# Performance work log

Measured on AMD Instinct MI355X. Metric: run time of the kernel, lower is better.

The kernel has to match this reference:

```python
import jax, jax.numpy as jnp
import numpy as np

H, HKV, DH = 32, 8, 128
ROPE_BASE = 500000.0


def _rope(x, pos):
    # x: [B, H, T, D]; MLX non-traditional rope (split halves)
    D = x.shape[-1]
    half = D // 2
    freqs = ROPE_BASE ** (-(jnp.arange(half, dtype=jnp.float32) * 2.0 / D))  # [half]
    t = pos + jnp.arange(x.shape[2], dtype=jnp.float32)                      # [T]
    ang = t[:, None] * freqs[None, :]                                        # [T, half]
    cos, sin = jnp.cos(ang), jnp.sin(ang)
    x1, x2 = x[..., :half], x[..., half:]
    return jnp.concatenate([x1 * cos - x2 * sin, x1 * sin + x2 * cos], axis=-1)


def setup_inputs() -> dict:
    key = jax.random.key(0)
    ks = jax.random.split(key, 5)
    B, T, HID = 1, 2048, 4096
    s = 0.02
    return {
        "hidden_states": jax.random.normal(ks[0], (B, T, HID), jnp.float32),
        "Wq": jax.random.normal(ks[1], (H * DH, HID), jnp.float32) * s,
        "Wk": jax.random.normal(ks[2], (HKV * DH, HID), jnp.float32) * s,
        "Wv": jax.random.normal(ks[3], (HKV * DH, HID), jnp.float32) * s,
        "Wo": jax.random.normal(ks[4], (HID, H * DH), jnp.float32) * s,
        "k_cache": jnp.zeros((1, HKV, 4096, DH), jnp.float32),
        "v_cache": jnp.zeros((1, HKV, 4096, DH), jnp.float32),
        "pos_int": 0,
    }


def reference(hidden_states, Wq, Wk, Wv, Wo, k_cache, v_cache, pos_int):
    B, T, _ = hidden_states.shape
    # QKV projections (no bias, Llama-style) -> [B, h, T, D]
    q = (hidden_states @ Wq.T).reshape(B, T, H, DH).transpose(0, 2, 1, 3)
    k = (hidden_states @ Wk.T).reshape(B, T, HKV, DH).transpose(0, 2, 1, 3)
    v = (hidden_states @ Wv.T).reshape(B, T, HKV, DH).transpose(0, 2, 1, 3)
    # RoPE with position offset
    q = _rope(q, pos_int)
    k = _rope(k, pos_int)
    # KV-cache scatter update at pos_int, then window to [:pos_int+T]
    k_cache = jax.lax.dynamic_update_slice(k_cache, k, (0, 0, pos_int, 0))
    v_cache = jax.lax.dynamic_update_slice(v_cache, v, (0, 0, pos_int, 0))
    Tk = pos_int + T
    k_win = k_cache[:, :, :Tk, :]
    v_win = v_cache[:, :, :Tk, :]
    # GQA: repeat_interleave KV heads to match query heads
    group = H // HKV
    k_ = jnp.repeat(k_win, group, axis=1)   # [B, H, Tk, D]
    v_ = jnp.repeat(v_win, group, axis=1)
    # SDPA, is_causal=True => top-left aligned causal mask (query i sees keys j<=i)
    scale = 1.0 / jnp.sqrt(jnp.asarray(DH, jnp.float32))
    scores = jnp.einsum("bhtd,bhsd->bhts", q, k_) * scale  # [B, H, T, Tk]
    causal = jnp.arange(Tk)[None, :] <= jnp.arange(T)[:, None]
    scores = jnp.where(causal[None, None], scores, jnp.finfo(scores.dtype).min)
    attn = jax.nn.softmax(scores, axis=-1)
    out = jnp.einsum("bhts,bhsd->bhtd", attn, v_)           # [B, H, T, D]
    out = out.transpose(0, 2, 1, 3).reshape(B, T, H * DH)
    return out @ Wo.T
```

## Files before the change

kernel.cpp:

```cpp
#include <hip/hip_runtime.h>


#define DEVI __device__ __forceinline__

typedef __attribute__((ext_vector_type(8))) short short8;
typedef __attribute__((ext_vector_type(4))) float f32x4;

DEVI unsigned short f2bf(float f) {
  union { float f; unsigned u; } x; x.f = f;
  unsigned r = x.u + 0x7FFFu + ((x.u >> 16) & 1u);
  return (unsigned short)(r >> 16);
}
DEVI float bf2f(unsigned short h) {
  union { unsigned u; float f; } x; x.u = ((unsigned)h) << 16;
  return x.f;
}
DEVI f32x4 mfma16(short8 a, short8 b, f32x4 c) {
  return __builtin_amdgcn_mfma_f32_16x16x32_bf16(a, b, c, 0, 0, 0);
}
DEVI void gl2lds16(const unsigned short* g, unsigned short* l) {
  __builtin_amdgcn_global_load_lds(
      (const __attribute__((address_space(1))) unsigned int*)g,
      (__attribute__((address_space(3))) unsigned int*)l, 16, 0, 0);
}
DEVI void bar() { __builtin_amdgcn_s_barrier(); }
DEVI void sfence() { __builtin_amdgcn_sched_barrier(0); }

__global__ __launch_bounds__(256)
void cvt_kernel(const float* __restrict__ src, unsigned short* __restrict__ dst,
                int n4) {
  int i = blockIdx.x * 256 + threadIdx.x;
  const int stride = gridDim.x * 256;
  for (; i < n4; i += stride) {
    float4 v = ((const float4*)src)[i];
    ushort4 h;
    h.x = f2bf(v.x); h.y = f2bf(v.y); h.z = f2bf(v.z); h.w = f2bf(v.w);
    ((ushort4*)dst)[i] = h;
  }
}

__global__ __launch_bounds__(512, 2)
void gemm_qkv_8ph(const unsigned short* __restrict__ hsb,
                  const unsigned short* __restrict__ Wqb,
                  const unsigned short* __restrict__ Wkb,
                  const unsigned short* __restrict__ Wvb,
                  unsigned short* __restrict__ Qb,
                  unsigned short* __restrict__ Kb,
                  unsigned short* __restrict__ Vb) {
  const int K = 4096;
  const int NT = 64;
  __shared__ __align__(16) unsigned short Ls[2][2][2][256][32];
  const int tid = threadIdx.x, lane = tid & 63, w = tid >> 6;
  const int wr = w >> 2, wc = w & 3;
  const int m0 = blockIdx.y * 256;
  const int n0g = blockIdx.x * 256;

  const unsigned short* Bsrc; unsigned short* outp; int ldo, oc;
  if (n0g < 4096)      { Bsrc = Wqb + (size_t)n0g * K;          outp = Qb; ldo = 4096; oc = n0g; }
  else if (n0g < 5120) { Bsrc = Wkb + (size_t)(n0g - 4096) * K; outp = Kb; ldo = 1024; oc = n0g - 4096; }
  else                 { Bsrc = Wvb + (size_t)(n0g - 5120) * K; outp = Vb; ldo = 1024; oc = n0g - 5120; }
  const unsigned short* Asrc = hsb + (size_t)m0 * K;

  auto stageU = [&](const unsigned short* src, int ab, int kh, int tt, int bb) {
#pragma unroll
    for (int j = 0; j < 2; ++j) {
      const int seg = j * 8 + w;
      const int row = seg * 16 + (lane >> 2);
      const int cs  = (lane & 3) ^ ((row >> 1) & 3);
      gl2lds16(src + (size_t)row * K + tt * 64 + kh * 32 + cs * 8,
               &Ls[bb][ab][kh][seg * 16][0]);
    }
  };
  auto ldA = [&](int bb, int kh, int fm) -> short8 {
    const int ra = wr * 128 + fm * 16 + (lane & 15);
    const int cs = (lane >> 4) ^ ((ra >> 1) & 3);
    return *(const short8*)&Ls[bb][0][kh][ra][cs * 8];
  };
  auto ldB = [&](int bb, int kh, int fn) -> short8 {
    const int rb = wc * 64 + fn * 16 + (lane & 15);
    const int cs = (lane >> 4) ^ ((rb >> 1) & 3);
    return *(const short8*)&Ls[bb][1][kh][rb][cs * 8];
  };

  f32x4 acc[8][4];
#pragma unroll
  for (int i = 0; i < 8; ++i)
#pragma unroll
    for (int j = 0; j < 4; ++j) acc[i][j] = (f32x4){0.f, 0.f, 0.f, 0.f};

  stageU(Asrc, 0, 0, 0, 0);
  stageU(Asrc, 0, 1, 0, 0);
  stageU(Bsrc, 1, 0, 0, 0);
  stageU(Bsrc, 1, 1, 0, 0);
  stageU(Bsrc, 1, 0, 1, 1);
  stageU(Asrc, 0, 0, 1, 1);
  stageU(Bsrc, 1, 1, 1, 1);
  asm volatile("s_waitcnt vmcnt(6)" ::: "memory");
  bar();
  sfence();

  short8 af[4], bfr[4];
  for (int t = 0; t < NT; ++t) {
    const int bb = t & 1, nb = bb ^ 1;
#pragma unroll
    for (int i = 0; i < 4; ++i) af[i] = ldA(bb, 0, i);
#pragma unroll
    for (int i = 0; i < 4; ++i) bfr[i] = ldB(bb, 0, i);
    if (t + 1 < NT) stageU(Asrc, 0, 1, t + 1, nb);
    bar();
    __builtin_amdgcn_s_setprio(1);
#pragma unroll
    for (int i = 0; i < 4; ++i)
#pragma unroll
      for (int j = 0; j < 4; ++j) acc[i][j] = mfma16(af[i], bfr[j], acc[i][j]);
    __builtin_amdgcn_s_setprio(0);
    sfence(); bar(); sfence();
#pragma unroll
    for (int i = 0; i < 4; ++i) af[i] = ldA(bb, 0, 4 + i);
    if (t + 2 < NT) stageU(Bsrc, 1, 0, t + 2, bb);
    bar();
    __builtin_amdgcn_s_setprio(1);
#pragma unroll
    for (int i = 0; i < 4; ++i)
#pragma unroll
      for (int j = 0; j < 4; ++j) acc[4 + i][j] = mfma16(af[i], bfr[j], acc[4 + i][j]);
    __builtin_amdgcn_s_setprio(0);
    sfence(); bar(); sfence();
#pragma unroll
    for (int i = 0; i < 4; ++i) af[i] = ldA(bb, 1, i);
#pragma unroll
    for (int i = 0; i < 4; ++i) bfr[i] = ldB(bb, 1, i);
    if (t + 2 < NT) stageU(Asrc, 0, 0, t + 2, bb);
    bar();
    __builtin_amdgcn_s_setprio(1);
#pragma unroll
    for (int i = 0; i < 4; ++i)
#pragma unroll
      for (int j = 0; j < 4; ++j) acc[i][j] = mfma16(af[i], bfr[j], acc[i][j]);
    __builtin_amdgcn_s_setprio(0);
    sfence(); bar(); sfence();
#pragma unroll
    for (int i = 0; i < 4; ++i) af[i] = ldA(bb, 1, 4 + i);
    if (t + 2 < NT) stageU(Bsrc, 1, 1, t + 2, bb);
    bar();
    __builtin_amdgcn_s_setprio(1);
#pragma unroll
    for (int i = 0; i < 4; ++i)
#pragma unroll
      for (int j = 0; j < 4; ++j) acc[4 + i][j] = mfma16(af[i], bfr[j], acc[4 + i][j]);
    __builtin_amdgcn_s_setprio(0);
    if (t < NT - 2) asm volatile("s_waitcnt vmcnt(6)" ::: "memory");
    else            asm volatile("s_waitcnt vmcnt(0)" ::: "memory");
    sfence(); bar(); sfence();
  }

#pragma unroll
  for (int fm = 0; fm < 8; ++fm) {
    const int rb0 = m0 + wr * 128 + fm * 16 + ((lane >> 4) << 2);
#pragma unroll
    for (int fn = 0; fn < 4; ++fn) {
      const int cb = oc + wc * 64 + fn * 16 + (lane & 15);
#pragma unroll
      for (int r = 0; r < 4; ++r)
        outp[(size_t)(rb0 + r) * ldo + cb] = f2bf(acc[fm][fn][r]);
    }
  }
}

__global__ __launch_bounds__(256)
void transpose_v(const unsigned short* __restrict__ Vb,
                 unsigned short* __restrict__ VtG) {
  __shared__ unsigned short tile[64][68];
  const int tid = threadIdx.x;
  const int t0 = blockIdx.x * 64;
  const int c0 = blockIdx.y * 64;
  const int r = tid >> 4;
  const int c4 = (tid & 15) << 2;
#pragma unroll
  for (int i = 0; i < 4; ++i) {
    ushort4 v = *(const ushort4*)(Vb + (size_t)(t0 + r + i * 16) * 1024 + c0 + c4);
    *(ushort4*)&tile[r + i * 16][c4] = v;
  }
  __syncthreads();
#pragma unroll
  for (int i = 0; i < 4; ++i) {
    int d = r + i * 16;
    ushort4 o;
    o.x = tile[c4 + 0][d]; o.y = tile[c4 + 1][d];
    o.z = tile[c4 + 2][d]; o.w = tile[c4 + 3][d];
    *(ushort4*)(VtG + (size_t)(c0 + d) * 2048 + t0 + c4) = o;
  }
}

__global__ __launch_bounds__(256)
void rope_kernel(unsigned short* __restrict__ Qb, unsigned short* __restrict__ Kb,
                 const int* __restrict__ posp) {
  const int QP = 2048 * 32 * 64;
  const int KP = 2048 * 8 * 64;
  int idx = blockIdx.x * 256 + threadIdx.x;
  if (idx >= QP + KP) return;
  unsigned short* base; int t, hh, d, ld;
  if (idx < QP) {
    base = Qb; ld = 4096;
    t = idx >> 11; int rem = idx & 2047; hh = rem >> 6; d = rem & 63;
  } else {
    int j = idx - QP; base = Kb; ld = 1024;
    t = j >> 9; int rem = j & 511; hh = rem >> 6; d = rem & 63;
  }
  float freq = exp2f(-(float)d * 0.29580575880077f);
  float ang = (float)(t + posp[0]) * freq;
  float s, c;
  __sincosf(ang, &s, &c);
  size_t i1 = (size_t)t * ld + hh * 128 + d;
  float x1 = bf2f(base[i1]), x2 = bf2f(base[i1 + 64]);
  base[i1]      = f2bf(x1 * c - x2 * s);
  base[i1 + 64] = f2bf(x1 * s + x2 * c);
}

__global__ __launch_bounds__(512, 4)
void attn_kernel(const unsigned short* __restrict__ Qb,
                 const unsigned short* __restrict__ Kb,
                 const unsigned short* __restrict__ VtG,
                 unsigned short* __restrict__ Ob) {
  __shared__ __align__(16) unsigned short Ks[64][128];
  __shared__ __align__(16) unsigned short Vt[128][64];
  __shared__ __align__(16) unsigned short Ps[8][16][64];
  const int tid = threadIdx.x, lane = tid & 63, w = tid >> 6;
  const int h = blockIdx.y;
  const int qt = (blockIdx.y >> 4) ? (15 - blockIdx.x) : blockIdx.x;
  const int kh = h >> 2;
  const int q0 = qt * 128;
  const float SCALE = 0.08838834764831845f;

  short8 aq[4];
  {
    const int qrow = q0 + w * 16 + (lane & 15);
#pragma unroll
    for (int ks = 0; ks < 4; ++ks)
      aq[ks] = *(const short8*)(Qb + (size_t)qrow * 4096 + h * 128 + ks * 32 +
                                ((lane >> 4) << 3));
  }

  f32x4 o_acc[8];
#pragma unroll
  for (int n8 = 0; n8 < 8; ++n8) o_acc[n8] = (f32x4){0.f, 0.f, 0.f, 0.f};
  float mst[4], lst[4];
#pragma unroll
  for (int r = 0; r < 4; ++r) { mst[r] = -1e30f; lst[r] = 0.f; }

  const int ksrow0 = w * 8 + (lane >> 4);
  const int vdrow0 = w * 16 + (lane >> 3);

  const int ntiles = 2 * (qt + 1);
  for (int st = 0; st < ntiles; ++st) {
    const int s0 = st * 64;
#pragma unroll
    for (int j = 0; j < 2; ++j) {
      int sr = ksrow0 + j * 4;
      int sc = (((lane & 15) << 4) ^ ((sr & 7) << 4)) >> 1;
      gl2lds16(Kb + (size_t)(s0 + sr) * 1024 + kh * 128 + sc, &Ks[w * 8 + j * 4][0]);
    }
#pragma unroll
    for (int j = 0; j < 2; ++j) {
      int dr = vdrow0 + j * 8;
      int sc = (((lane & 7) << 4) ^ ((dr & 7) << 4)) >> 1;
      gl2lds16(VtG + (size_t)(kh * 128 + dr) * 2048 + s0 + sc, &Vt[w * 16 + j * 8][0]);
    }
    __syncthreads();

    f32x4 sacc[4];
#pragma unroll
    for (int ni = 0; ni < 4; ++ni) sacc[ni] = (f32x4){0.f, 0.f, 0.f, 0.f};
#pragma unroll
    for (int ks = 0; ks < 4; ++ks) {
      const int co = ks * 64 + ((lane >> 4) << 4);
      short8 bk[4];
#pragma unroll
      for (int ni = 0; ni < 4; ++ni) {
        int kr = ni * 16 + (lane & 15);
        bk[ni] = *(const short8*)((const char*)(&Ks[kr][0]) + (co ^ ((kr & 7) << 4)));
      }
#pragma unroll
      for (int ni = 0; ni < 4; ++ni)
        sacc[ni] = mfma16(aq[ks], bk[ni], sacc[ni]);
    }

    char* pb = (char*)(&Ps[w][0][0]);
#pragma unroll
    for (int r = 0; r < 4; ++r) {
      const int qrow = q0 + w * 16 + ((lane >> 4) << 2) + r;
      float v4[4]; float vmax = -1e30f;
#pragma unroll
      for (int ni = 0; ni < 4; ++ni) {
        int scol = s0 + ni * 16 + (lane & 15);
        float x = sacc[ni][r] * SCALE;
        if (scol > qrow) x = -1e30f;
        v4[ni] = x; vmax = fmaxf(vmax, x);
      }
      vmax = fmaxf(vmax, __shfl_xor(vmax, 1));
      vmax = fmaxf(vmax, __shfl_xor(vmax, 2));
      vmax = fmaxf(vmax, __shfl_xor(vmax, 4));
      vmax = fmaxf(vmax, __shfl_xor(vmax, 8));
      float mo = mst[r];
      float mn = fmaxf(mo, vmax);
      float al = __expf(mo - mn);
      float rs = 0.f;
      const int prow = ((lane >> 4) << 2) + r;
      const int pswz = ((prow >> 2) & 3) << 5;
#pragma unroll
      for (int ni = 0; ni < 4; ++ni) {
        float p = __expf(v4[ni] - mn);
        rs += p;
        int cbyte = (ni * 16 + (lane & 15)) * 2;
        *(unsigned short*)(pb + prow * 128 + (cbyte ^ pswz)) = f2bf(p);
      }
      rs += __shfl_xor(rs, 1);
      rs += __shfl_xor(rs, 2);
      rs += __shfl_xor(rs, 4);
      rs += __shfl_xor(rs, 8);
      lst[r] = lst[r] * al + rs;
      mst[r] = mn;
#pragma unroll
      for (int n8 = 0; n8 < 8; ++n8) o_acc[n8][r] *= al;
    }

#pragma unroll
    for (int ks2 = 0; ks2 < 2; ++ks2) {
      const int co = ks2 * 64 + ((lane >> 4) << 4);
      const int pr = lane & 15;
      short8 pa = *(const short8*)(pb + pr * 128 + (co ^ (((pr >> 2) & 3) << 5)));
#pragma unroll
      for (int n8 = 0; n8 < 8; ++n8) {
        int vr = n8 * 16 + (lane & 15);
        short8 bv = *(const short8*)((const char*)(&Vt[vr][0]) + (co ^ ((vr & 7) << 4)));
        o_acc[n8] = mfma16(pa, bv, o_acc[n8]);
      }
    }
    __syncthreads();
  }

#pragma unroll
  for (int r = 0; r < 4; ++r) {
    float inv = 1.0f / lst[r];
    int row = q0 + w * 16 + ((lane >> 4) << 2) + r;
#pragma unroll
    for (int n8 = 0; n8 < 8; ++n8)
      Ob[(size_t)row * 4096 + h * 128 + n8 * 16 + (lane & 15)] =
          f2bf(o_acc[n8][r] * inv);
  }
}

__global__ __launch_bounds__(256, 2)
void gemm_out_bf16(const unsigned short* __restrict__ Ab,
                   const unsigned short* __restrict__ Wob,
                   float* __restrict__ Cout) {
  const int K = 4096;
  __shared__ __align__(16) unsigned short As[128][64];
  __shared__ __align__(16) unsigned short Bs[128][64];
  const int tid = threadIdx.x, lane = tid & 63, wid = tid >> 6;
  const int m0 = blockIdx.y * 128;
  const int n0 = blockIdx.x * 128;
  const unsigned short* Asrc = Ab + (size_t)m0 * K;
  const unsigned short* Bsrc = Wob + (size_t)n0 * K;

  f32x4 acc[4][4];
#pragma unroll
  for (int i = 0; i < 4; ++i)
#pragma unroll
    for (int j = 0; j < 4; ++j) acc[i][j] = (f32x4){0.f, 0.f, 0.f, 0.f};

  const int wm = (wid >> 1) * 64, wn = (wid & 1) * 64;
  const int srow = wid * 32 + (lane >> 3);
  const int scol = (lane & 7) * 8;

  for (int k0 = 0; k0 < K; k0 += 64) {
#pragma unroll
    for (int i = 0; i < 4; ++i) {
      gl2lds16(Asrc + (size_t)(srow + i * 8) * K + k0 + scol, &As[wid * 32 + i * 8][0]);
      gl2lds16(Bsrc + (size_t)(srow + i * 8) * K + k0 + scol, &Bs[wid * 32 + i * 8][0]);
    }
    __syncthreads();
#pragma unroll
    for (int ks = 0; ks < 2; ++ks) {
      short8 af[4], bfr[4];
      const int co = ks * 64 + ((lane >> 4) << 4);
#pragma unroll
      for (int i = 0; i < 4; ++i) {
        af[i]  = *(const short8*)((const char*)(&As[wm + i * 16 + (lane & 15)][0]) + co);
        bfr[i] = *(const short8*)((const char*)(&Bs[wn + i * 16 + (lane & 15)][0]) + co);
      }
#pragma unroll
      for (int i = 0; i < 4; ++i)
#pragma unroll
        for (int j = 0; j < 4; ++j)
          acc[i][j] = mfma16(af[i], bfr[j], acc[i][j]);
    }
    __syncthreads();
  }

#pragma unroll
  for (int i = 0; i < 4; ++i) {
    int rb = m0 + wm + i * 16 + ((lane >> 4) << 2);
#pragma unroll
    for (int j = 0; j < 4; ++j) {
      int cb = n0 + wn + j * 16 + (lane & 15);
#pragma unroll
      for (int r = 0; r < 4; ++r)
        Cout[(size_t)(rb + r) * 4096 + cb] = acc[i][j][r];
    }
  }
}

extern "C" void kernel_launch(void* const* d_in, const int* in_sizes, int n_in,
                              void* d_out, int out_size, void* d_ws, size_t ws_size,
                              hipStream_t stream) {
  const float* hs = (const float*)d_in[0];
  const float* Wq = (const float*)d_in[1];
  const float* Wk = (const float*)d_in[2];
  const float* Wv = (const float*)d_in[3];
  const float* Wo = (const float*)d_in[4];
  const int* pos = (const int*)d_in[7];

  unsigned short* hsb = (unsigned short*)d_ws;
  unsigned short* Wqb = hsb + (size_t)8  * 1024 * 1024;
  unsigned short* Wkb = Wqb + (size_t)16 * 1024 * 1024;
  unsigned short* Wvb = Wkb + (size_t)4  * 1024 * 1024;
  unsigned short* Wob = Wvb + (size_t)4  * 1024 * 1024;
  unsigned short* Qb  = Wob + (size_t)16 * 1024 * 1024;
  unsigned short* Kb  = Qb  + (size_t)8  * 1024 * 1024;
  unsigned short* Vb  = Kb  + (size_t)2  * 1024 * 1024;
  unsigned short* Ob  = Vb  + (size_t)2  * 1024 * 1024;
  unsigned short* VtG = hsb;
  float* out = (float*)d_out;

  cvt_kernel<<<dim3(2048), 256, 0, stream>>>(hs, hsb, 2 * 1024 * 1024);
  cvt_kernel<<<dim3(2048), 256, 0, stream>>>(Wq, Wqb, 4 * 1024 * 1024);
  cvt_kernel<<<dim3(1024), 256, 0, stream>>>(Wk, Wkb, 1 * 1024 * 1024);
  cvt_kernel<<<dim3(1024), 256, 0, stream>>>(Wv, Wvb, 1 * 1024 * 1024);
  cvt_kernel<<<dim3(2048), 256, 0, stream>>>(Wo, Wob, 4 * 1024 * 1024);

  gemm_qkv_8ph<<<dim3(24, 8), 512, 0, stream>>>(hsb, Wqb, Wkb, Wvb, Qb, Kb, Vb);
  transpose_v<<<dim3(32, 16), 256, 0, stream>>>(Vb, VtG);
  const int npairs = 2048 * 32 * 64 + 2048 * 8 * 64;
  rope_kernel<<<dim3((npairs + 255) / 256), 256, 0, stream>>>(Qb, Kb, pos);
  attn_kernel<<<dim3(16, 32), 512, 0, stream>>>(Qb, Kb, VtG, Ob);
  gemm_out_bf16<<<dim3(32, 16), 256, 0, stream>>>(Ob, Wob, out);
}
```

Baseline: 367.4 us.

## Widen attention KV tile to 128 and fuse conversion and post-GEMM launches

The attention kernel now processes 128 keys per iteration instead of 64. That halves the number of loop trips and the barriers per query tile, and doubles the MFMA work between synchronisations. The five fp32-to-bf16 conversion launches are merged into one kernel, and the V transpose and RoPE kernels are merged into a single launch, to cut launch and tail overhead. The trade-off is attention LDS growing to about 96KB per block, with the occupancy hint of 4 removed. That likely limits residency to one block per CU and raises register pressure from the larger score arrays.

```diff
diff --git a/kernel.cpp b/kernel.cpp
--- a/kernel.cpp
+++ b/kernel.cpp
@@ -26,17 +26,31 @@
 DEVI void bar() { __builtin_amdgcn_s_barrier(); }
 DEVI void sfence() { __builtin_amdgcn_sched_barrier(0); }
 
-__global__ __launch_bounds__(256)
-void cvt_kernel(const float* __restrict__ src, unsigned short* __restrict__ dst,
-                int n4) {
-  int i = blockIdx.x * 256 + threadIdx.x;
-  const int stride = gridDim.x * 256;
-  for (; i < n4; i += stride) {
+DEVI void cvt_region(const float* __restrict__ src,
+                     unsigned short* __restrict__ dst, int n4, int start,
+                     int stride) {
+  for (int i = start; i < n4; i += stride) {
     float4 v = ((const float4*)src)[i];
     ushort4 h;
     h.x = f2bf(v.x); h.y = f2bf(v.y); h.z = f2bf(v.z); h.w = f2bf(v.w);
     ((ushort4*)dst)[i] = h;
   }
+}
+__global__ __launch_bounds__(256)
+void cvt5_kernel(const float* __restrict__ s0, const float* __restrict__ s1,
+                 const float* __restrict__ s2, const float* __restrict__ s3,
+                 const float* __restrict__ s4,
+                 unsigned short* __restrict__ d0, unsigned short* __restrict__ d1,
+                 unsigned short* __restrict__ d2, unsigned short* __restrict__ d3,
+                 unsigned short* __restrict__ d4,
+                 int n0, int n1, int n2, int n3, int n4) {
+  const int start = blockIdx.x * 256 + threadIdx.x;
+  const int stride = gridDim.x * 256;
+  cvt_region(s0, d0, n0, start, stride);
+  cvt_region(s1, d1, n1, start, stride);
+  cvt_region(s2, d2, n2, start, stride);
+  cvt_region(s3, d3, n3, start, stride);
+  cvt_region(s4, d4, n4, start, stride);
 }
 
 __global__ __launch_bounds__(512, 2)
@@ -168,36 +182,37 @@
 }
 
 __global__ __launch_bounds__(256)
-void transpose_v(const unsigned short* __restrict__ Vb,
-                 unsigned short* __restrict__ VtG) {
+void postproc_kernel(const unsigned short* __restrict__ Vb,
+                     unsigned short* __restrict__ VtG,
+                     unsigned short* __restrict__ Qb,
+                     unsigned short* __restrict__ Kb,
+                     const int* __restrict__ posp) {
   __shared__ unsigned short tile[64][68];
-  const int tid = threadIdx.x;
-  const int t0 = blockIdx.x * 64;
-  const int c0 = blockIdx.y * 64;
-  const int r = tid >> 4;
-  const int c4 = (tid & 15) << 2;
-#pragma unroll
-  for (int i = 0; i < 4; ++i) {
-    ushort4 v = *(const ushort4*)(Vb + (size_t)(t0 + r + i * 16) * 1024 + c0 + c4);
-    *(ushort4*)&tile[r + i * 16][c4] = v;
-  }
-  __syncthreads();
-#pragma unroll
-  for (int i = 0; i < 4; ++i) {
-    int d = r + i * 16;
-    ushort4 o;
-    o.x = tile[c4 + 0][d]; o.y = tile[c4 + 1][d];
-    o.z = tile[c4 + 2][d]; o.w = tile[c4 + 3][d];
-    *(ushort4*)(VtG + (size_t)(c0 + d) * 2048 + t0 + c4) = o;
-  }
-}
-
-__global__ __launch_bounds__(256)
-void rope_kernel(unsigned short* __restrict__ Qb, unsigned short* __restrict__ Kb,
-                 const int* __restrict__ posp) {
+  const int b = blockIdx.x, tid = threadIdx.x;
+  if (b < 512) {
+    const int t0 = (b & 31) * 64;
+    const int c0 = (b >> 5) * 64;
+    const int r = tid >> 4;
+    const int c4 = (tid & 15) << 2;
+#pragma unroll
+    for (int i = 0; i < 4; ++i) {
+      ushort4 v = *(const ushort4*)(Vb + (size_t)(t0 + r + i * 16) * 1024 + c0 + c4);
+      *(ushort4*)&tile[r + i * 16][c4] = v;
+    }
+    __syncthreads();
+#pragma unroll
+    for (int i = 0; i < 4; ++i) {
+      int d = r + i * 16;
+      ushort4 o;
+      o.x = tile[c4 + 0][d]; o.y = tile[c4 + 1][d];
+      o.z = tile[c4 + 2][d]; o.w = tile[c4 + 3][d];
+      *(ushort4*)(VtG + (size_t)(c0 + d) * 2048 + t0 + c4) = o;
+    }
+    return;
+  }
   const int QP = 2048 * 32 * 64;
   const int KP = 2048 * 8 * 64;
-  int idx = blockIdx.x * 256 + threadIdx.x;
+  int idx = (b - 512) * 256 + tid;
   if (idx >= QP + KP) return;
   unsigned short* base; int t, hh, d, ld;
   if (idx < QP) {
@@ -217,14 +232,14 @@
   base[i1 + 64] = f2bf(x1 * s + x2 * c);
 }
 
-__global__ __launch_bounds__(512, 4)
+__global__ __launch_bounds__(512)
 void attn_kernel(const unsigned short* __restrict__ Qb,
                  const unsigned short* __restrict__ Kb,
                  const unsigned short* __restrict__ VtG,
                  unsigned short* __restrict__ Ob) {
-  __shared__ __align__(16) unsigned short Ks[64][128];
-  __shared__ __align__(16) unsigned short Vt[128][64];
-  __shared__ __align__(16) unsigned short Ps[8][16][64];
+  __shared__ __align__(16) unsigned short Ks[128][128];
+  __shared__ __align__(16) unsigned short Vt[128][128];
+  __shared__ __align__(16) unsigned short Ps[8][16][128];
   const int tid = threadIdx.x, lane = tid & 63, w = tid >> 6;
   const int h = blockIdx.y;
   const int qt = (blockIdx.y >> 4) ? (15 - blockIdx.x) : blockIdx.x;
@@ -248,40 +263,37 @@
 #pragma unroll
   for (int r = 0; r < 4; ++r) { mst[r] = -1e30f; lst[r] = 0.f; }
 
-  const int ksrow0 = w * 8 + (lane >> 4);
-  const int vdrow0 = w * 16 + (lane >> 3);
-
-  const int ntiles = 2 * (qt + 1);
+  const int ntiles = qt + 1;
   for (int st = 0; st < ntiles; ++st) {
-    const int s0 = st * 64;
-#pragma unroll
-    for (int j = 0; j < 2; ++j) {
-      int sr = ksrow0 + j * 4;
+    const int s0 = st * 128;
+#pragma unroll
+    for (int j = 0; j < 4; ++j) {
+      int sr = w * 16 + j * 4 + (lane >> 4);
       int sc = (((lane & 15) << 4) ^ ((sr & 7) << 4)) >> 1;
-      gl2lds16(Kb + (size_t)(s0 + sr) * 1024 + kh * 128 + sc, &Ks[w * 8 + j * 4][0]);
-    }
-#pragma unroll
-    for (int j = 0; j < 2; ++j) {
-      int dr = vdrow0 + j * 8;
-      int sc = (((lane & 7) << 4) ^ ((dr & 7) << 4)) >> 1;
-      gl2lds16(VtG + (size_t)(kh * 128 + dr) * 2048 + s0 + sc, &Vt[w * 16 + j * 8][0]);
+      gl2lds16(Kb + (size_t)(s0 + sr) * 1024 + kh * 128 + sc, &Ks[w * 16 + j * 4][0]);
+    }
+#pragma unroll
+    for (int j = 0; j < 4; ++j) {
+      int dr = w * 16 + j * 4 + (lane >> 4);
+      int sc = (((lane & 15) << 4) ^ ((dr & 7) << 4)) >> 1;
+      gl2lds16(VtG + (size_t)(kh * 128 + dr) * 2048 + s0 + sc, &Vt[w * 16 + j * 4][0]);
     }
     __syncthreads();
 
-    f32x4 sacc[4];
-#pragma unroll
-    for (int ni = 0; ni < 4; ++ni) sacc[ni] = (f32x4){0.f, 0.f, 0.f, 0.f};
+    f32x4 sacc[8];
+#pragma unroll
+    for (int ni = 0; ni < 8; ++ni) sacc[ni] = (f32x4){0.f, 0.f, 0.f, 0.f};
 #pragma unroll
     for (int ks = 0; ks < 4; ++ks) {
       const int co = ks * 64 + ((lane >> 4) << 4);
-      short8 bk[4];
-#pragma unroll
-      for (int ni = 0; ni < 4; ++ni) {
+      short8 bk[8];
+#pragma unroll
+      for (int ni = 0; ni < 8; ++ni) {
         int kr = ni * 16 + (lane & 15);
         bk[ni] = *(const short8*)((const char*)(&Ks[kr][0]) + (co ^ ((kr & 7) << 4)));
       }
 #pragma unroll
-      for (int ni = 0; ni < 4; ++ni)
+      for (int ni = 0; ni < 8; ++ni)
         sacc[ni] = mfma16(aq[ks], bk[ni], sacc[ni]);
     }
 
@@ -289,13 +301,13 @@
 #pragma unroll
     for (int r = 0; r < 4; ++r) {
       const int qrow = q0 + w * 16 + ((lane >> 4) << 2) + r;
-      float v4[4]; float vmax = -1e30f;
-#pragma unroll
-      for (int ni = 0; ni < 4; ++ni) {
+      float v8[8]; float vmax = -1e30f;
+#pragma unroll
+      for (int ni = 0; ni < 8; ++ni) {
         int scol = s0 + ni * 16 + (lane & 15);
         float x = sacc[ni][r] * SCALE;
         if (scol > qrow) x = -1e30f;
-        v4[ni] = x; vmax = fmaxf(vmax, x);
+        v8[ni] = x; vmax = fmaxf(vmax, x);
       }
       vmax = fmaxf(vmax, __shfl_xor(vmax, 1));
       vmax = fmaxf(vmax, __shfl_xor(vmax, 2));
@@ -308,11 +320,11 @@
       const int prow = ((lane >> 4) << 2) + r;
       const int pswz = ((prow >> 2) & 3) << 5;
 #pragma unroll
-      for (int ni = 0; ni < 4; ++ni) {
-        float p = __expf(v4[ni] - mn);
+      for (int ni = 0; ni < 8; ++ni) {
+        float p = __expf(v8[ni] - mn);
         rs += p;
         int cbyte = (ni * 16 + (lane & 15)) * 2;
-        *(unsigned short*)(pb + prow * 128 + (cbyte ^ pswz)) = f2bf(p);
+        *(unsigned short*)(pb + prow * 256 + (cbyte ^ pswz)) = f2bf(p);
       }
       rs += __shfl_xor(rs, 1);
       rs += __shfl_xor(rs, 2);
@@ -325,10 +337,10 @@
     }
 
 #pragma unroll
-    for (int ks2 = 0; ks2 < 2; ++ks2) {
+    for (int ks2 = 0; ks2 < 4; ++ks2) {
       const int co = ks2 * 64 + ((lane >> 4) << 4);
       const int pr = lane & 15;
-      short8 pa = *(const short8*)(pb + pr * 128 + (co ^ (((pr >> 2) & 3) << 5)));
+      short8 pa = *(const short8*)(pb + pr * 256 + (co ^ (((pr >> 2) & 3) << 5)));
 #pragma unroll
       for (int n8 = 0; n8 < 8; ++n8) {
         int vr = n8 * 16 + (lane & 15);
@@ -433,16 +445,17 @@
   unsigned short* VtG = hsb;
   float* out = (float*)d_out;
 
-  cvt_kernel<<<dim3(2048), 256, 0, stream>>>(hs, hsb, 2 * 1024 * 1024);
-  cvt_kernel<<<dim3(2048), 256, 0, stream>>>(Wq, Wqb, 4 * 1024 * 1024);
-  cvt_kernel<<<dim3(1024), 256, 0, stream>>>(Wk, Wkb, 1 * 1024 * 1024);
-  cvt_kernel<<<dim3(1024), 256, 0, stream>>>(Wv, Wvb, 1 * 1024 * 1024);
-  cvt_kernel<<<dim3(2048), 256, 0, stream>>>(Wo, Wob, 4 * 1024 * 1024);
+  cvt5_kernel<<<dim3(2048), 256, 0, stream>>>(
+      hs, Wq, Wk, Wv, Wo, hsb, Wqb, Wkb, Wvb, Wob,
+      2 * 1024 * 1024, 4 * 1024 * 1024, 1 * 1024 * 1024, 1 * 1024 * 1024,
+      4 * 1024 * 1024);
 
   gemm_qkv_8ph<<<dim3(24, 8), 512, 0, stream>>>(hsb, Wqb, Wkb, Wvb, Qb, Kb, Vb);
-  transpose_v<<<dim3(32, 16), 256, 0, stream>>>(Vb, VtG);
+
   const int npairs = 2048 * 32 * 64 + 2048 * 8 * 64;
-  rope_kernel<<<dim3((npairs + 255) / 256), 256, 0, stream>>>(Qb, Kb, pos);
+  const int rope_blocks = (npairs + 255) / 256;
+  postproc_kernel<<<dim3(512 + rope_blocks), 256, 0, stream>>>(Vb, VtG, Qb, Kb, pos);
+
   attn_kernel<<<dim3(16, 32), 512, 0, stream>>>(Qb, Kb, VtG, Ob);
   gemm_out_bf16<<<dim3(32, 16), 256, 0, stream>>>(Ob, Wob, out);
 }
```

Result: no change. 366.9 us (-0.1%).
